# Performance work log

Hardware: AMD Instinct MI355X
Metric: run time of the kernel (lower is better)

Reference implementation:

```python
import jax, jax.numpy as jnp
import numpy as np

N = 20000      # nodes
E = 320000     # edges (avg degree 16)
F = 128        # feature_size
H = 3          # gat_conv_num_head
NEG_SLOPE = 0.2


def gat_layer(x, W, attn_l, attn_r, bias, src, dst, n, heads, out):
    """DGL-style GATConv: proj -> per-edge LeakyReLU scores -> edge softmax over
    incoming edges of each destination node -> scatter-sum aggregate + bias."""
    h = (x @ W).reshape(n, heads, out)                 # [N, H, F]
    el = jnp.sum(h * attn_l, axis=-1)                  # [N, H]  a_l . h
    er = jnp.sum(h * attn_r, axis=-1)                  # [N, H]  a_r . h
    e = jax.nn.leaky_relu(el[src] + er[dst], NEG_SLOPE)  # [E, H]
    # numerically stable softmax over edges grouped by destination node
    emax = jax.ops.segment_max(e, dst, num_segments=n)   # [N, H]
    a = jnp.exp(e - emax[dst])                           # [E, H]
    denom = jax.ops.segment_sum(a, dst, num_segments=n)  # [N, H]
    alpha = a / denom[dst]                               # [E, H]
    rst = jax.ops.segment_sum(alpha[:, :, None] * h[src], dst, num_segments=n)  # [N, H, F]
    return rst + bias.reshape(1, heads, out)


def setup_inputs() -> dict:
    key = jax.random.key(0)
    ks = jax.random.split(key, 10)
    feats = jax.random.normal(ks[0], (N, F), dtype=jnp.float32)
    src = jax.random.randint(ks[1], (E,), 0, N)
    # guarantee every node has >=1 incoming edge (allow_zero_in_degree=False)
    dst = jnp.concatenate([jnp.arange(N), jax.random.randint(ks[2], (E - N,), 0, N)])
    s = 0.08  # ~xavier scale for fan 128
    W1 = jax.random.normal(ks[3], (F, H * F), dtype=jnp.float32) * s
    attn_l1 = jax.random.normal(ks[4], (H, F), dtype=jnp.float32) * s
    attn_r1 = jax.random.normal(ks[5], (H, F), dtype=jnp.float32) * s
    bias1 = jnp.zeros((H * F,), dtype=jnp.float32)
    W2 = jax.random.normal(ks[6], (H * F, F), dtype=jnp.float32) * 0.05
    attn_l2 = jax.random.normal(ks[7], (1, F), dtype=jnp.float32) * s
    attn_r2 = jax.random.normal(ks[8], (1, F), dtype=jnp.float32) * s
    bias2 = jnp.zeros((F,), dtype=jnp.float32)
    return {"feats": feats, "W1": W1, "attn_l1": attn_l1, "attn_r1": attn_r1,
            "bias1": bias1, "W2": W2, "attn_l2": attn_l2, "attn_r2": attn_r2,
            "bias2": bias2, "src": src, "dst": dst}


def reference(feats, W1, attn_l1, attn_r1, bias1, W2, attn_l2, attn_r2, bias2, src, dst):
    h = gat_layer(feats, W1, attn_l1, attn_r1, bias1, src, dst, N, H, F)  # [N, 3, 128]
    h = h.reshape(N, H * F)                                               # [N, 384]
    out = gat_layer(h, W2, attn_l2, attn_r2, bias2, src, dst, N, 1, F)    # [N, 1, 128]
    return out
```

## Files before the change

kernel.cpp:

```cpp
#include <hip/hip_runtime.h>
#include <hip/hip_bf16.h>

#define N_NODES 20000
#define N_EDGES 320000
#define NEG_SLOPE 0.2f

__device__ __forceinline__ unsigned int bf16pack(float a, float b) {
    unsigned int ua = __float_as_uint(a);
    ua = (ua + 0x7fffu + ((ua >> 16) & 1u)) >> 16;
    unsigned int ub = __float_as_uint(b);
    ub = (ub + 0x7fffu + ((ub >> 16) & 1u)) >> 16;
    return ua | (ub << 16);
}

__global__ void hist_kernel(const int* __restrict__ dst, int* __restrict__ deg) {
    int e = blockIdx.x * blockDim.x + threadIdx.x;
    if (e < N_EDGES) atomicAdd(&deg[dst[e]], 1);
}

__global__ __launch_bounds__(1024) void scan_kernel(const int* __restrict__ deg,
                                                    int* __restrict__ offsets,
                                                    int* __restrict__ pos) {
    __shared__ int sums[1024];
    const int CH = (N_NODES + 1023) / 1024;
    int t = threadIdx.x;
    int beg = t * CH;
    int end = min(beg + CH, N_NODES);
    int loc[20];
    int s = 0;
    for (int i = beg; i < end; ++i) { loc[i - beg] = s; s += deg[i]; }
    sums[t] = s;
    __syncthreads();
    for (int st = 1; st < 1024; st <<= 1) {
        int v = (t >= st) ? sums[t - st] : 0;
        __syncthreads();
        sums[t] += v;
        __syncthreads();
    }
    int excl = (t == 0) ? 0 : sums[t - 1];
    for (int i = beg; i < end; ++i) {
        int o = excl + loc[i - beg];
        offsets[i] = o;
        pos[i] = o;
    }
    if (t == 1023) offsets[N_NODES] = sums[1023];
}

__global__ void scatter_kernel(const int* __restrict__ src, const int* __restrict__ dst,
                               int* __restrict__ pos, int* __restrict__ elist) {
    int e = blockIdx.x * blockDim.x + threadIdx.x;
    if (e < N_EDGES) {
        int p = atomicAdd(&pos[dst[e]], 1);
        elist[p] = src[e];
    }
}

__global__ __launch_bounds__(256) void gemm1_kernel(const float* __restrict__ X,
                                                    const float* __restrict__ W,
                                                    const float* __restrict__ al,
                                                    const float* __restrict__ ar,
                                                    uint2* __restrict__ H1b,
                                                    float* __restrict__ EL,
                                                    float* __restrict__ ER) {
    __shared__ float xsT[128][36];
    int tid = threadIdx.x;
    int tm = tid >> 5;
    int tn = tid & 31;
    int row0 = blockIdx.x * 32;
    int head = blockIdx.y;
    int n0 = head * 128;

#pragma unroll
    for (int j = 0; j < 4; ++j) {
        int idx = tid + j * 256;
        int m = idx >> 5, k4 = idx & 31;
        float4 v = *(const float4*)&X[(size_t)(row0 + m) * 128 + k4 * 4];
        xsT[k4 * 4 + 0][m] = v.x;
        xsT[k4 * 4 + 1][m] = v.y;
        xsT[k4 * 4 + 2][m] = v.z;
        xsT[k4 * 4 + 3][m] = v.w;
    }
    __syncthreads();

    float acc[4][4] = {};
    const float* Wp = W + n0 + tn * 4;
#pragma unroll 4
    for (int k = 0; k < 128; ++k) {
        float4 w = *(const float4*)&Wp[(size_t)k * 384];
        float4 x = *(const float4*)&xsT[k][tm * 4];
        float xv[4] = {x.x, x.y, x.z, x.w};
        float wv[4] = {w.x, w.y, w.z, w.w};
#pragma unroll
        for (int r = 0; r < 4; ++r)
#pragma unroll
            for (int c = 0; c < 4; ++c) acc[r][c] = fmaf(xv[r], wv[c], acc[r][c]);
    }

    float4 av = *(const float4*)&al[n0 + tn * 4];
    float4 rv = *(const float4*)&ar[n0 + tn * 4];
    float avv[4] = {av.x, av.y, av.z, av.w};
    float rvv[4] = {rv.x, rv.y, rv.z, rv.w};
#pragma unroll
    for (int r = 0; r < 4; ++r) {
        int row = row0 + tm * 4 + r;
        uint2 pk;
        pk.x = bf16pack(acc[r][0], acc[r][1]);
        pk.y = bf16pack(acc[r][2], acc[r][3]);
        H1b[(size_t)row * 96 + head * 32 + tn] = pk;
        float vl = acc[r][0] * avv[0] + acc[r][1] * avv[1] + acc[r][2] * avv[2] + acc[r][3] * avv[3];
        float vr = acc[r][0] * rvv[0] + acc[r][1] * rvv[1] + acc[r][2] * rvv[2] + acc[r][3] * rvv[3];
#pragma unroll
        for (int s = 16; s > 0; s >>= 1) {
            vl += __shfl_down(vl, s, 32);
            vr += __shfl_down(vr, s, 32);
        }
        if (tn == 0) {
            EL[row * 3 + head] = vl;
            ER[row * 3 + head] = vr;
        }
    }
}

__global__ __launch_bounds__(256) void gemm2_kernel(const float* __restrict__ X2,
                                                    const float* __restrict__ W,
                                                    const float* __restrict__ al,
                                                    const float* __restrict__ ar,
                                                    float* __restrict__ H2,
                                                    float* __restrict__ EL,
                                                    float* __restrict__ ER) {
    __shared__ float xsT[128][36];
    int tid = threadIdx.x;
    int tm = tid >> 5;
    int tn = tid & 31;
    int row0 = blockIdx.x * 32;

    float acc[4][4] = {};
    for (int c = 0; c < 3; ++c) {
#pragma unroll
        for (int j = 0; j < 4; ++j) {
            int idx = tid + j * 256;
            int m = idx >> 5, k4 = idx & 31;
            float4 v = *(const float4*)&X2[(size_t)(row0 + m) * 384 + c * 128 + k4 * 4];
            xsT[k4 * 4 + 0][m] = v.x;
            xsT[k4 * 4 + 1][m] = v.y;
            xsT[k4 * 4 + 2][m] = v.z;
            xsT[k4 * 4 + 3][m] = v.w;
        }
        __syncthreads();
        const float* Wp = W + (size_t)c * 128 * 128 + tn * 4;
#pragma unroll 4
        for (int k = 0; k < 128; ++k) {
            float4 w = *(const float4*)&Wp[(size_t)k * 128];
            float4 x = *(const float4*)&xsT[k][tm * 4];
            float xv[4] = {x.x, x.y, x.z, x.w};
            float wv[4] = {w.x, w.y, w.z, w.w};
#pragma unroll
            for (int r = 0; r < 4; ++r)
#pragma unroll
                for (int cc = 0; cc < 4; ++cc) acc[r][cc] = fmaf(xv[r], wv[cc], acc[r][cc]);
        }
        __syncthreads();
    }

    float4 av = *(const float4*)&al[tn * 4];
    float4 rv = *(const float4*)&ar[tn * 4];
    float avv[4] = {av.x, av.y, av.z, av.w};
    float rvv[4] = {rv.x, rv.y, rv.z, rv.w};
#pragma unroll
    for (int r = 0; r < 4; ++r) {
        int row = row0 + tm * 4 + r;
        float4 o = make_float4(acc[r][0], acc[r][1], acc[r][2], acc[r][3]);
        *(float4*)&H2[(size_t)row * 128 + tn * 4] = o;
        float vl = acc[r][0] * avv[0] + acc[r][1] * avv[1] + acc[r][2] * avv[2] + acc[r][3] * avv[3];
        float vr = acc[r][0] * rvv[0] + acc[r][1] * rvv[1] + acc[r][2] * rvv[2] + acc[r][3] * rvv[3];
#pragma unroll
        for (int s = 16; s > 0; s >>= 1) {
            vl += __shfl_down(vl, s, 32);
            vr += __shfl_down(vr, s, 32);
        }
        if (tn == 0) {
            EL[row] = vl;
            ER[row] = vr;
        }
    }
}

__global__ __launch_bounds__(192) void agg1_kernel(const unsigned int* __restrict__ H1b,
                                                   const float* __restrict__ EL,
                                                   const float* __restrict__ ER,
                                                   const int* __restrict__ offsets,
                                                   const int* __restrict__ elist,
                                                   const float* __restrict__ bias,
                                                   float* __restrict__ OUT) {
    __shared__ int s_src[128];
    __shared__ float s_sc[3][128];
    __shared__ float s_w[3][128];
    int n = blockIdx.x;
    int t = threadIdx.x;
    int hd = t >> 6;
    int q  = t & 63;
    int o0 = offsets[n], o1 = offsets[n + 1];
    int deg = o1 - o0;
    float er0 = ER[n * 3 + 0], er1v = ER[n * 3 + 1], er2v = ER[n * 3 + 2];
    float m = -1e30f, l = 0.f, alo = 0.f, ahi = 0.f;
    for (int base = 0; base < deg; base += 128) {
        int cnt = min(128, deg - base);
        if (t < cnt) {
            int s = elist[o0 + base + t];
            s_src[t] = s;
            float e0 = EL[s * 3 + 0] + er0;
            float e1 = EL[s * 3 + 1] + er1v;
            float e2 = EL[s * 3 + 2] + er2v;
            s_sc[0][t] = e0 > 0.f ? e0 : NEG_SLOPE * e0;
            s_sc[1][t] = e1 > 0.f ? e1 : NEG_SLOPE * e1;
            s_sc[2][t] = e2 > 0.f ? e2 : NEG_SLOPE * e2;
        }
        __syncthreads();
        float nm = m;
        for (int i = 0; i < cnt; ++i) nm = fmaxf(nm, s_sc[hd][i]);
        float f = __expf(m - nm);
        alo *= f; ahi *= f; l *= f;
        m = nm;
        if (q < cnt)      s_w[hd][q]      = __expf(s_sc[hd][q] - m);
        if (q + 64 < cnt) s_w[hd][q + 64] = __expf(s_sc[hd][q + 64] - m);
        __syncthreads();
        for (int i = 0; i < cnt; ++i) {
            float w = s_w[hd][i];
            l += w;
            unsigned int v = H1b[(size_t)s_src[i] * 192 + hd * 64 + q];
            float lo = __uint_as_float(v << 16);
            float hi = __uint_as_float(v & 0xffff0000u);
            alo = fmaf(w, lo, alo);
            ahi = fmaf(w, hi, ahi);
        }
        __syncthreads();
    }
    int fo = n * 384 + hd * 128 + 2 * q;
    OUT[fo]     = alo / l + bias[hd * 128 + 2 * q];
    OUT[fo + 1] = ahi / l + bias[hd * 128 + 2 * q + 1];
}

__global__ __launch_bounds__(128) void agg2_kernel(const float* __restrict__ H2,
                                                   const float* __restrict__ EL,
                                                   const float* __restrict__ ER,
                                                   const int* __restrict__ offsets,
                                                   const int* __restrict__ elist,
                                                   const float* __restrict__ bias,
                                                   float* __restrict__ OUT) {
    __shared__ int s_src[128];
    __shared__ float s_sc[128];
    __shared__ float s_w[128];
    int n = blockIdx.x;
    int t = threadIdx.x;
    int o0 = offsets[n], o1 = offsets[n + 1];
    int deg = o1 - o0;
    float ern = ER[n];
    float m = -1e30f, l = 0.f, a = 0.f;
    for (int base = 0; base < deg; base += 128) {
        int cnt = min(128, deg - base);
        if (t < cnt) {
            int s = elist[o0 + base + t];
            s_src[t] = s;
            float e = EL[s] + ern;
            s_sc[t] = e > 0.f ? e : NEG_SLOPE * e;
        }
        __syncthreads();
        float nm = m;
        for (int i = 0; i < cnt; ++i) nm = fmaxf(nm, s_sc[i]);
        float fct = __expf(m - nm);
        a *= fct; l *= fct; m = nm;
        if (t < cnt) s_w[t] = __expf(s_sc[t] - m);
        __syncthreads();
        for (int i = 0; i < cnt; ++i) {
            float w = s_w[i];
            l += w;
            a += w * H2[(size_t)s_src[i] * 128 + t];
        }
        __syncthreads();
    }
    OUT[(size_t)n * 128 + t] = a / l + bias[t];
}

extern "C" void kernel_launch(void* const* d_in, const int* in_sizes, int n_in,
                              void* d_out, int out_size, void* d_ws, size_t ws_size,
                              hipStream_t stream) {
    const float* feats = (const float*)d_in[0];
    const float* W1    = (const float*)d_in[1];
    const float* al1   = (const float*)d_in[2];
    const float* ar1   = (const float*)d_in[3];
    const float* b1    = (const float*)d_in[4];
    const float* W2    = (const float*)d_in[5];
    const float* al2   = (const float*)d_in[6];
    const float* ar2   = (const float*)d_in[7];
    const float* b2    = (const float*)d_in[8];
    const int* src     = (const int*)d_in[9];
    const int* dst     = (const int*)d_in[10];
    float* out = (float*)d_out;

    char* ws = (char*)d_ws;
    size_t off = 0;
    auto alloc = [&](size_t bytes) {
        void* p = ws + off;
        off += (bytes + 255) & ~(size_t)255;
        return p;
    };
    unsigned int* h1b = (unsigned int*)alloc((size_t)N_NODES * 192 * 4);
    float* x2  = (float*)alloc((size_t)N_NODES * 384 * 4);
    float* el1 = (float*)alloc((size_t)N_NODES * 3 * 4);
    float* er1 = (float*)alloc((size_t)N_NODES * 3 * 4);
    float* el2 = (float*)alloc((size_t)N_NODES * 4);
    float* er2 = (float*)alloc((size_t)N_NODES * 4);
    int* deg     = (int*)alloc((size_t)N_NODES * 4);
    int* offsets = (int*)alloc((size_t)(N_NODES + 1) * 4);
    int* pos     = (int*)alloc((size_t)N_NODES * 4);
    int* elist   = (int*)alloc((size_t)N_EDGES * 4);
    float* h2 = (float*)h1b;

    hipMemsetAsync(deg, 0, (size_t)N_NODES * 4, stream);
    hist_kernel<<<(N_EDGES + 255) / 256, 256, 0, stream>>>(dst, deg);
    scan_kernel<<<1, 1024, 0, stream>>>(deg, offsets, pos);
    scatter_kernel<<<(N_EDGES + 255) / 256, 256, 0, stream>>>(src, dst, pos, elist);

    dim3 g1(N_NODES / 32, 3);
    gemm1_kernel<<<g1, 256, 0, stream>>>(feats, W1, al1, ar1, (uint2*)h1b, el1, er1);
    agg1_kernel<<<N_NODES, 192, 0, stream>>>(h1b, el1, er1, offsets, elist, b1, x2);
    dim3 g2(N_NODES / 32, 1);
    gemm2_kernel<<<g2, 256, 0, stream>>>(x2, W2, al2, ar2, h2, el2, er2);
    agg2_kernel<<<N_NODES, 128, 0, stream>>>(h2, el2, er2, offsets, elist, b2, out);
}
```

Measured before the change: 299.3 us.

## Store layer-2 projection as bf16 and shrink GEMM tiles to 16 rows

The layer-2 projection is now stored as packed bf16, and agg2 uses 64 threads per node that each handle two features, which halves the gather traffic in the second aggregation. Both GEMMs move from 32-row to 16-row tiles with a row-major shared-memory tile instead of a transposed one. This doubles the number of blocks for the 20000-row problem but cuts per-thread reuse of weight loads. The agg outputs are written as float2 stores. Storing H2 in bf16 adds rounding error to the second layer.

```diff
diff --git a/kernel.cpp b/kernel.cpp
--- a/kernel.cpp
+++ b/kernel.cpp
@@ -62,38 +62,40 @@
                                                     uint2* __restrict__ H1b,
                                                     float* __restrict__ EL,
                                                     float* __restrict__ ER) {
-    __shared__ float xsT[128][36];
+    __shared__ float xs[16][132];
     int tid = threadIdx.x;
     int tm = tid >> 5;
     int tn = tid & 31;
-    int row0 = blockIdx.x * 32;
+    int row0 = blockIdx.x * 16;
     int head = blockIdx.y;
     int n0 = head * 128;
 
 #pragma unroll
-    for (int j = 0; j < 4; ++j) {
+    for (int j = 0; j < 2; ++j) {
         int idx = tid + j * 256;
         int m = idx >> 5, k4 = idx & 31;
-        float4 v = *(const float4*)&X[(size_t)(row0 + m) * 128 + k4 * 4];
-        xsT[k4 * 4 + 0][m] = v.x;
-        xsT[k4 * 4 + 1][m] = v.y;
-        xsT[k4 * 4 + 2][m] = v.z;
-        xsT[k4 * 4 + 3][m] = v.w;
+        *(float4*)&xs[m][k4 * 4] = *(const float4*)&X[(size_t)(row0 + m) * 128 + k4 * 4];
     }
     __syncthreads();
 
-    float acc[4][4] = {};
+    int ra = tm * 2, rb = ra + 1;
+    float acc[2][4] = {};
     const float* Wp = W + n0 + tn * 4;
-#pragma unroll 4
-    for (int k = 0; k < 128; ++k) {
-        float4 w = *(const float4*)&Wp[(size_t)k * 384];
-        float4 x = *(const float4*)&xsT[k][tm * 4];
-        float xv[4] = {x.x, x.y, x.z, x.w};
-        float wv[4] = {w.x, w.y, w.z, w.w};
-#pragma unroll
-        for (int r = 0; r < 4; ++r)
-#pragma unroll
-            for (int c = 0; c < 4; ++c) acc[r][c] = fmaf(xv[r], wv[c], acc[r][c]);
+    for (int k4 = 0; k4 < 32; ++k4) {
+        float4 xa = *(const float4*)&xs[ra][k4 * 4];
+        float4 xb = *(const float4*)&xs[rb][k4 * 4];
+        float xav[4] = {xa.x, xa.y, xa.z, xa.w};
+        float xbv[4] = {xb.x, xb.y, xb.z, xb.w};
+#pragma unroll
+        for (int kk = 0; kk < 4; ++kk) {
+            float4 w = *(const float4*)&Wp[(size_t)(k4 * 4 + kk) * 384];
+            float wv[4] = {w.x, w.y, w.z, w.w};
+#pragma unroll
+            for (int c = 0; c < 4; ++c) {
+                acc[0][c] = fmaf(xav[kk], wv[c], acc[0][c]);
+                acc[1][c] = fmaf(xbv[kk], wv[c], acc[1][c]);
+            }
+        }
     }
 
     float4 av = *(const float4*)&al[n0 + tn * 4];
@@ -101,8 +103,8 @@
     float avv[4] = {av.x, av.y, av.z, av.w};
     float rvv[4] = {rv.x, rv.y, rv.z, rv.w};
 #pragma unroll
-    for (int r = 0; r < 4; ++r) {
-        int row = row0 + tm * 4 + r;
+    for (int r = 0; r < 2; ++r) {
+        int row = row0 + ra + r;
         uint2 pk;
         pk.x = bf16pack(acc[r][0], acc[r][1]);
         pk.y = bf16pack(acc[r][2], acc[r][3]);
@@ -125,39 +127,42 @@
                                                     const float* __restrict__ W,
                                                     const float* __restrict__ al,
                                                     const float* __restrict__ ar,
-                                                    float* __restrict__ H2,
+                                                    uint2* __restrict__ H2b,
                                                     float* __restrict__ EL,
                                                     float* __restrict__ ER) {
-    __shared__ float xsT[128][36];
+    __shared__ float xs[16][132];
     int tid = threadIdx.x;
     int tm = tid >> 5;
     int tn = tid & 31;
-    int row0 = blockIdx.x * 32;
-
-    float acc[4][4] = {};
+    int row0 = blockIdx.x * 16;
+    int ra = tm * 2, rb = ra + 1;
+
+    float acc[2][4] = {};
     for (int c = 0; c < 3; ++c) {
 #pragma unroll
-        for (int j = 0; j < 4; ++j) {
+        for (int j = 0; j < 2; ++j) {
             int idx = tid + j * 256;
             int m = idx >> 5, k4 = idx & 31;
-            float4 v = *(const float4*)&X2[(size_t)(row0 + m) * 384 + c * 128 + k4 * 4];
-            xsT[k4 * 4 + 0][m] = v.x;
-            xsT[k4 * 4 + 1][m] = v.y;
-            xsT[k4 * 4 + 2][m] = v.z;
-            xsT[k4 * 4 + 3][m] = v.w;
+            *(float4*)&xs[m][k4 * 4] =
+                *(const float4*)&X2[(size_t)(row0 + m) * 384 + c * 128 + k4 * 4];
         }
         __syncthreads();
         const float* Wp = W + (size_t)c * 128 * 128 + tn * 4;
-#pragma unroll 4
-        for (int k = 0; k < 128; ++k) {
-            float4 w = *(const float4*)&Wp[(size_t)k * 128];
-            float4 x = *(const float4*)&xsT[k][tm * 4];
-            float xv[4] = {x.x, x.y, x.z, x.w};
-            float wv[4] = {w.x, w.y, w.z, w.w};
-#pragma unroll
-            for (int r = 0; r < 4; ++r)
-#pragma unroll
-                for (int cc = 0; cc < 4; ++cc) acc[r][cc] = fmaf(xv[r], wv[cc], acc[r][cc]);
+        for (int k4 = 0; k4 < 32; ++k4) {
+            float4 xa = *(const float4*)&xs[ra][k4 * 4];
+            float4 xb = *(const float4*)&xs[rb][k4 * 4];
+            float xav[4] = {xa.x, xa.y, xa.z, xa.w};
+            float xbv[4] = {xb.x, xb.y, xb.z, xb.w};
+#pragma unroll
+            for (int kk = 0; kk < 4; ++kk) {
+                float4 w = *(const float4*)&Wp[(size_t)(k4 * 4 + kk) * 128];
+                float wv[4] = {w.x, w.y, w.z, w.w};
+#pragma unroll
+                for (int cc = 0; cc < 4; ++cc) {
+                    acc[0][cc] = fmaf(xav[kk], wv[cc], acc[0][cc]);
+                    acc[1][cc] = fmaf(xbv[kk], wv[cc], acc[1][cc]);
+                }
+            }
         }
         __syncthreads();
     }
@@ -167,10 +172,12 @@
     float avv[4] = {av.x, av.y, av.z, av.w};
     float rvv[4] = {rv.x, rv.y, rv.z, rv.w};
 #pragma unroll
-    for (int r = 0; r < 4; ++r) {
-        int row = row0 + tm * 4 + r;
-        float4 o = make_float4(acc[r][0], acc[r][1], acc[r][2], acc[r][3]);
-        *(float4*)&H2[(size_t)row * 128 + tn * 4] = o;
+    for (int r = 0; r < 2; ++r) {
+        int row = row0 + ra + r;
+        uint2 pk;
+        pk.x = bf16pack(acc[r][0], acc[r][1]);
+        pk.y = bf16pack(acc[r][2], acc[r][3]);
+        H2b[(size_t)row * 32 + tn] = pk;
         float vl = acc[r][0] * avv[0] + acc[r][1] * avv[1] + acc[r][2] * avv[2] + acc[r][3] * avv[3];
         float vr = acc[r][0] * rvv[0] + acc[r][1] * rvv[1] + acc[r][2] * rvv[2] + acc[r][3] * rvv[3];
 #pragma unroll
@@ -191,7 +198,7 @@
                                                    const int* __restrict__ offsets,
                                                    const int* __restrict__ elist,
                                                    const float* __restrict__ bias,
-                                                   float* __restrict__ OUT) {
+                                                   float2* __restrict__ OUT2) {
     __shared__ int s_src[128];
     __shared__ float s_sc[3][128];
     __shared__ float s_w[3][128];
@@ -235,18 +242,17 @@
         }
         __syncthreads();
     }
-    int fo = n * 384 + hd * 128 + 2 * q;
-    OUT[fo]     = alo / l + bias[hd * 128 + 2 * q];
-    OUT[fo + 1] = ahi / l + bias[hd * 128 + 2 * q + 1];
-}
-
-__global__ __launch_bounds__(128) void agg2_kernel(const float* __restrict__ H2,
-                                                   const float* __restrict__ EL,
-                                                   const float* __restrict__ ER,
-                                                   const int* __restrict__ offsets,
-                                                   const int* __restrict__ elist,
-                                                   const float* __restrict__ bias,
-                                                   float* __restrict__ OUT) {
+    int b0 = hd * 128 + 2 * q;
+    OUT2[(size_t)n * 192 + hd * 64 + q] = make_float2(alo / l + bias[b0], ahi / l + bias[b0 + 1]);
+}
+
+__global__ __launch_bounds__(64) void agg2_kernel(const unsigned int* __restrict__ H2b,
+                                                  const float* __restrict__ EL,
+                                                  const float* __restrict__ ER,
+                                                  const int* __restrict__ offsets,
+                                                  const int* __restrict__ elist,
+                                                  const float* __restrict__ bias,
+                                                  float2* __restrict__ OUT2) {
     __shared__ int s_src[128];
     __shared__ float s_sc[128];
     __shared__ float s_w[128];
@@ -255,30 +261,35 @@
     int o0 = offsets[n], o1 = offsets[n + 1];
     int deg = o1 - o0;
     float ern = ER[n];
-    float m = -1e30f, l = 0.f, a = 0.f;
+    float m = -1e30f, l = 0.f, alo = 0.f, ahi = 0.f;
     for (int base = 0; base < deg; base += 128) {
         int cnt = min(128, deg - base);
-        if (t < cnt) {
-            int s = elist[o0 + base + t];
-            s_src[t] = s;
+        for (int u = t; u < cnt; u += 64) {
+            int s = elist[o0 + base + u];
+            s_src[u] = s;
             float e = EL[s] + ern;
-            s_sc[t] = e > 0.f ? e : NEG_SLOPE * e;
+            s_sc[u] = e > 0.f ? e : NEG_SLOPE * e;
         }
         __syncthreads();
         float nm = m;
         for (int i = 0; i < cnt; ++i) nm = fmaxf(nm, s_sc[i]);
-        float fct = __expf(m - nm);
-        a *= fct; l *= fct; m = nm;
-        if (t < cnt) s_w[t] = __expf(s_sc[t] - m);
+        float f = __expf(m - nm);
+        alo *= f; ahi *= f; l *= f;
+        m = nm;
+        for (int u = t; u < cnt; u += 64) s_w[u] = __expf(s_sc[u] - m);
         __syncthreads();
         for (int i = 0; i < cnt; ++i) {
             float w = s_w[i];
             l += w;
-            a += w * H2[(size_t)s_src[i] * 128 + t];
-        }
-        __syncthreads();
-    }
-    OUT[(size_t)n * 128 + t] = a / l + bias[t];
+            unsigned int v = H2b[(size_t)s_src[i] * 64 + t];
+            float lo = __uint_as_float(v << 16);
+            float hi = __uint_as_float(v & 0xffff0000u);
+            alo = fmaf(w, lo, alo);
+            ahi = fmaf(w, hi, ahi);
+        }
+        __syncthreads();
+    }
+    OUT2[(size_t)n * 64 + t] = make_float2(alo / l + bias[2 * t], ahi / l + bias[2 * t + 1]);
 }
 
 extern "C" void kernel_launch(void* const* d_in, const int* in_sizes, int n_in,
@@ -314,17 +325,16 @@
     int* offsets = (int*)alloc((size_t)(N_NODES + 1) * 4);
     int* pos     = (int*)alloc((size_t)N_NODES * 4);
     int* elist   = (int*)alloc((size_t)N_EDGES * 4);
-    float* h2 = (float*)h1b;
+    unsigned int* h2b = h1b;
 
     hipMemsetAsync(deg, 0, (size_t)N_NODES * 4, stream);
     hist_kernel<<<(N_EDGES + 255) / 256, 256, 0, stream>>>(dst, deg);
     scan_kernel<<<1, 1024, 0, stream>>>(deg, offsets, pos);
     scatter_kernel<<<(N_EDGES + 255) / 256, 256, 0, stream>>>(src, dst, pos, elist);
 
-    dim3 g1(N_NODES / 32, 3);
+    dim3 g1(N_NODES / 16, 3);
     gemm1_kernel<<<g1, 256, 0, stream>>>(feats, W1, al1, ar1, (uint2*)h1b, el1, er1);
-    agg1_kernel<<<N_NODES, 192, 0, stream>>>(h1b, el1, er1, offsets, elist, b1, x2);
-    dim3 g2(N_NODES / 32, 1);
-    gemm2_kernel<<<g2, 256, 0, stream>>>(x2, W2, al2, ar2, h2, el2, er2);
-    agg2_kernel<<<N_NODES, 128, 0, stream>>>(h2, el2, er2, offsets, elist, b2, out);
-}
+    agg1_kernel<<<N_NODES, 192, 0, stream>>>(h1b, el1, er1, offsets, elist, b1, (float2*)x2);
+    gemm2_kernel<<<N_NODES / 16, 256, 0, stream>>>(x2, W2, al2, ar2, (uint2*)h2b, el2, er2);
+    agg2_kernel<<<N_NODES, 64, 0, stream>>>(h2b, el2, er2, offsets, elist, b2, (float2*)out);
+}
```

After: 323.6 us. 1.08x slower.
